# Kernel tuning notes

Hardware: AMD Instinct MI355X
Metric: run time of the kernel (lower is better)

Reference implementation:

```python
import jax, jax.numpy as jnp
import numpy as np


def setup_inputs() -> dict:
    key = jax.random.key(0)
    k1, k2, k3 = jax.random.split(key, 3)
    B, d, N, T = 8, 256, 4096, 1024
    K = jax.random.normal(k1, (B, d, N), dtype=jnp.float32)
    V = jax.random.normal(k2, (B, d, N), dtype=jnp.float32)
    Q = jax.random.normal(k3, (B, d, T), dtype=jnp.float32)
    return {"K": K, "V": V, "Q": Q}


def reference(K, V, Q):
    d = K.shape[1]
    scale = 1.0 / jnp.sqrt(jnp.asarray(d, dtype=K.dtype))
    # scores: (B, N, T) = K^T @ Q
    scores = jnp.einsum('bdn,bdt->bnt', K, Q) * scale
    A = jax.nn.softmax(scores, axis=1)  # softmax over keys N
    R = jnp.einsum('bdn,bnt->bdt', V, A)  # (B, d, T)
    R_ = jnp.concatenate((R, Q), axis=1)  # (B, 2d, T)
    maxAtt = jnp.argmax(A, axis=1)  # (B, T)
    return (R_, A, maxAtt)
```

## Files before the change

### kernel.cpp

```cpp
#include <hip/hip_runtime.h>
#include <cfloat>

#define BB 8
#define DD 256
#define NN 4096
#define TT 1024
constexpr float SCALE = 0.0625f;

typedef __attribute__((ext_vector_type(8))) short bf16x8;
typedef __attribute__((ext_vector_type(4))) float f32x4;
typedef __attribute__((ext_vector_type(8))) unsigned short u16x8;

__device__ inline unsigned short f2bf(float x) {
  union { float f; unsigned u; } v; v.f = x;
  unsigned r = v.u + 0x7fff + ((v.u >> 16) & 1);
  return (unsigned short)(r >> 16);
}
__device__ inline float bf2f(unsigned short h) {
  union { unsigned u; float f; } v; v.u = ((unsigned)h) << 16;
  return v.f;
}

__device__ inline void glds16(const unsigned short* g, const short* lbase) {
  __builtin_amdgcn_global_load_lds((const __attribute__((address_space(1))) unsigned int*)g,
                                   (__attribute__((address_space(3))) unsigned int*)lbase,
                                   16, 0, 0);
}

__device__ inline void wg_barrier() {
  __builtin_amdgcn_sched_barrier(0);
  __builtin_amdgcn_s_barrier();
  __builtin_amdgcn_sched_barrier(0);
}

#define MPART_OFF 0u
#define LPART_OFF (1u << 20)
#define IPART_OFF (2u << 20)
#define MARR_OFF  (3u << 20)
#define RLARR_OFF ((3u << 20) + 32768u)
#define CONV_OFF  (4u << 20)
#define KT_HI_OFF (CONV_OFF)
#define KT_LO_OFF (CONV_OFF + 16777216u)
#define QT_HI_OFF (CONV_OFF + 33554432u)
#define QT_LO_OFF (CONV_OFF + 37748736u)
#define VH_OFF    (CONV_OFF + 41943040u)
#define RPART_OFF (CONV_OFF)
#define WS_NEED   (62914560ull)

__global__ __launch_bounds__(256) void convert_t2(const float* __restrict__ Ksrc,
                                                  const float* __restrict__ Qsrc,
                                                  unsigned short* __restrict__ KHi,
                                                  unsigned short* __restrict__ KLo,
                                                  unsigned short* __restrict__ QHi,
                                                  unsigned short* __restrict__ QLo) {
  __shared__ float tile[64][65];
  const int bx = blockIdx.x;
  const int b = blockIdx.z, d0 = blockIdx.y * 64;
  const float* src; unsigned short* dhi; unsigned short* dlo; int C; int c0;
  if (bx < 64) { src = Ksrc; dhi = KHi; dlo = KLo; C = NN; c0 = bx * 64; }
  else         { src = Qsrc; dhi = QHi; dlo = QLo; C = TT; c0 = (bx - 64) * 64; }
  const int tid = threadIdx.x;
  const float* s = src + ((size_t)b * DD + d0) * C + c0;
  const int r = tid >> 4, cg = (tid & 15) * 4;
#pragma unroll
  for (int it = 0; it < 4; ++it) {
    float4 v = *(const float4*)(s + (size_t)(r + it * 16) * C + cg);
    tile[r + it * 16][cg + 0] = v.x; tile[r + it * 16][cg + 1] = v.y;
    tile[r + it * 16][cg + 2] = v.z; tile[r + it * 16][cg + 3] = v.w;
  }
  __syncthreads();
  const int cl = tid >> 2, dg = (tid & 3) * 16;
  unsigned short hi[16], lo[16];
#pragma unroll
  for (int j = 0; j < 16; ++j) {
    float x = tile[dg + j][cl];
    unsigned short h = f2bf(x);
    hi[j] = h;
    lo[j] = f2bf(x - bf2f(h));
  }
  size_t off = ((size_t)b * C + c0 + cl) * DD + d0 + dg;
  *(u16x8*)(dhi + off) = *(u16x8*)&hi[0];
  *(u16x8*)(dhi + off + 8) = *(u16x8*)&hi[8];
  *(u16x8*)(dlo + off) = *(u16x8*)&lo[0];
  *(u16x8*)(dlo + off + 8) = *(u16x8*)&lo[8];
}

__global__ __launch_bounds__(256) void convert_v(const float* __restrict__ src,
                                                 unsigned short* __restrict__ dhi) {
  size_t g = (size_t)blockIdx.x * 256 + threadIdx.x;
  float4 v = ((const float4*)src)[g];
  unsigned short h[4] = {f2bf(v.x), f2bf(v.y), f2bf(v.z), f2bf(v.w)};
  *(ushort4*)(dhi + g * 4) = *(ushort4*)h;
}

__global__ __launch_bounds__(256) void gemm_scores_mfma(const unsigned short* __restrict__ KtHi,
                                                        const unsigned short* __restrict__ KtLo,
                                                        const unsigned short* __restrict__ QtHi,
                                                        const unsigned short* __restrict__ QtLo,
                                                        float* __restrict__ S,
                                                        float* __restrict__ mPart,
                                                        float* __restrict__ lPart,
                                                        int* __restrict__ iPart) {
  __shared__ __align__(16) short sAhi[128 * 32];
  __shared__ __align__(16) short sAlo[128 * 32];
  __shared__ __align__(16) short sBhi[128 * 32];
  __shared__ __align__(16) short sBlo[128 * 32];
  __shared__ float sm[256], sl[256];
  __shared__ int si[256];

  const int lin = blockIdx.x + ((blockIdx.y + (blockIdx.z << 5)) << 3);
  const int wg = ((lin & 7) << 8) + (lin >> 3);
  const int b = wg >> 8;
  const int cy = (wg >> 3) & 31;
  const int n0 = cy * 128;
  const int t0 = (wg & 7) * 128;
  const int tid = threadIdx.x;
  const int lane = tid & 63, w = tid >> 6;
  const int nh = (w & 1) * 64, th = (w >> 1) * 64;
  const int fr = lane & 15, q = lane >> 4;

  const unsigned short* aHi = KtHi + ((size_t)b * NN + n0) * DD;
  const unsigned short* aLo = KtLo + ((size_t)b * NN + n0) * DD;
  const unsigned short* bHi = QtHi + ((size_t)b * TT + t0) * DD;
  const unsigned short* bLo = QtLo + ((size_t)b * TT + t0) * DD;

  f32x4 acc[4][4];
#pragma unroll
  for (int i = 0; i < 4; ++i)
#pragma unroll
    for (int j = 0; j < 4; ++j) acc[i][j] = (f32x4){0.f, 0.f, 0.f, 0.f};

  const int R = lane >> 2;
  const int Qq = (lane & 3) ^ ((lane >> 3) & 3);
  const size_t s0 = (size_t)((w * 2 + 0) * 16 + R) * DD + Qq * 8;
  const size_t s1 = (size_t)((w * 2 + 1) * 16 + R) * DD + Qq * 8;
  const int d0 = (w * 2 + 0) * 512;
  const int d1 = (w * 2 + 1) * 512;
  const int pq8 = (q ^ ((fr >> 1) & 3)) * 8;

  for (int kk = 0; kk < DD; kk += 32) {
    glds16(aHi + s0 + kk, sAhi + d0);
    glds16(aHi + s1 + kk, sAhi + d1);
    glds16(aLo + s0 + kk, sAlo + d0);
    glds16(aLo + s1 + kk, sAlo + d1);
    glds16(bHi + s0 + kk, sBhi + d0);
    glds16(bHi + s1 + kk, sBhi + d1);
    glds16(bLo + s0 + kk, sBlo + d0);
    glds16(bLo + s1 + kk, sBlo + d1);
    __syncthreads();

    bf16x8 bh[4], bl[4];
#pragma unroll
    for (int tb = 0; tb < 4; ++tb) {
      int off = (((w >> 1) * 4 + tb) * 512) + fr * 32 + pq8;
      bh[tb] = *(const bf16x8*)&sBhi[off];
      bl[tb] = *(const bf16x8*)&sBlo[off];
    }
#pragma unroll
    for (int mb = 0; mb < 4; ++mb) {
      int off = (((w & 1) * 4 + mb) * 512) + fr * 32 + pq8;
      bf16x8 ah = *(const bf16x8*)&sAhi[off];
      bf16x8 al = *(const bf16x8*)&sAlo[off];
#pragma unroll
      for (int tb = 0; tb < 4; ++tb) {
        acc[mb][tb] = __builtin_amdgcn_mfma_f32_16x16x32_bf16(ah, bh[tb], acc[mb][tb], 0, 0, 0);
        acc[mb][tb] = __builtin_amdgcn_mfma_f32_16x16x32_bf16(ah, bl[tb], acc[mb][tb], 0, 0, 0);
        acc[mb][tb] = __builtin_amdgcn_mfma_f32_16x16x32_bf16(al, bh[tb], acc[mb][tb], 0, 0, 0);
      }
    }
    __syncthreads();
  }

#pragma unroll
  for (int tb = 0; tb < 4; ++tb) {
    const int tl = th + tb * 16 + fr;
    const int t = t0 + tl;
    float tmp[16];
    float m = -FLT_MAX; int id = 0;
#pragma unroll
    for (int mb = 0; mb < 4; ++mb)
#pragma unroll
      for (int r = 0; r < 4; ++r) {
        float v = acc[mb][tb][r] * SCALE;
        int n = n0 + nh + mb * 16 + q * 4 + r;
        S[((size_t)b * NN + n) * TT + t] = v;
        tmp[mb * 4 + r] = v;
        int nl = nh + mb * 16 + q * 4 + r;
        if (v > m) { m = v; id = nl; }
      }
    float l = 0.f;
#pragma unroll
    for (int j = 0; j < 16; ++j) l += __expf(tmp[j] - m);
#pragma unroll
    for (int off = 16; off <= 32; off <<= 1) {
      float m2 = __shfl_xor(m, off);
      float l2 = __shfl_xor(l, off);
      int i2 = __shfl_xor(id, off);
      if (m2 > m)       { l = l * __expf(m - m2) + l2; m = m2; id = i2; }
      else if (m2 == m) { l += l2; id = min(id, i2); }
      else              { l += l2 * __expf(m2 - m); }
    }
    if (q == 0) {
      int slot = (w & 1) * 128 + tl;
      sm[slot] = m; sl[slot] = l; si[slot] = id;
    }
  }
  __syncthreads();
  if (tid < 128) {
    float m = sm[tid], l = sl[tid]; int id = si[tid];
    float m2 = sm[128 + tid], l2 = sl[128 + tid]; int i2 = si[128 + tid];
    if (m2 > m)       { l = l * __expf(m - m2) + l2; m = m2; id = i2; }
    else if (m2 == m) { l += l2; id = min(id, i2); }
    else              { l += l2 * __expf(m2 - m); }
    size_t p = ((size_t)b * 32 + cy) * TT + t0 + tid;
    mPart[p] = m; lPart[p] = l; iPart[p] = n0 + id;
  }
}

__global__ __launch_bounds__(256) void gemm_out_fused2(const unsigned short* __restrict__ Vh,
                                                       float* __restrict__ A,
                                                       const float* __restrict__ mPart,
                                                       const float* __restrict__ lPart,
                                                       const int* __restrict__ iPart,
                                                       float* __restrict__ Rpart,
                                                       float* __restrict__ outMax) {
  __shared__ __align__(16) short sV[2][256 * 32];
  __shared__ __align__(16) short sA[32 * 40];
  __shared__ float rsm[8][32], rsl[8][32];
  __shared__ int   rsi[8][32];
  __shared__ float sm[32], srl[32];

  const int lin = blockIdx.x + (blockIdx.y << 5) + (blockIdx.z << 7);
  const int b  = lin & 7;
  const int ny = (lin >> 3) & 3;
  const int t0 = ((lin >> 5) & 31) * 32;

  const int tid = threadIdx.x;
  const int lane = tid & 63, w = tid >> 6;
  const int fr = lane & 15, q = lane >> 4, fk = q * 8;
  const int sn = tid >> 3, tg = tid & 7;

  const unsigned short* Vb = Vh + (size_t)b * DD * NN;
  float* Ab = A + (size_t)b * NN * TT;
  float* Arow = Ab + (size_t)sn * TT + t0 + tg * 4;

  const int R = lane >> 2;
  const int Qq = (lane & 3) ^ ((lane >> 3) & 3);
  const unsigned short* vsrc = Vb + (size_t)(w * 64 + R) * NN + Qq * 8;
  const int pq8 = (q ^ ((fr >> 1) & 3)) * 8;
  const int n0 = ny * 1024;

#pragma unroll
  for (int c = 0; c < 4; ++c)
    glds16(vsrc + (size_t)(c * 16) * NN + n0, &sV[0][(w * 4 + c) * 512]);
  float4 cur = *(const float4*)(Arow + (size_t)n0 * TT);

  {
    const int tl = tid & 31, g = tid >> 5;
    float m = -FLT_MAX, l = 0.f; int idx = 0;
#pragma unroll
    for (int cc = 0; cc < 4; ++cc) {
      size_t p = ((size_t)b * 32 + g * 4 + cc) * TT + t0 + tl;
      float m2 = mPart[p], l2 = lPart[p]; int i2 = iPart[p];
      if (m2 > m)       { l = l * __expf(m - m2) + l2; m = m2; idx = i2; }
      else if (m2 == m) { l += l2; idx = min(idx, i2); }
      else              { l += l2 * __expf(m2 - m); }
    }
    rsm[g][tl] = m; rsl[g][tl] = l; rsi[g][tl] = idx;
  }
  __syncthreads();
  if (tid < 32) {
    float m = rsm[0][tid], l = rsl[0][tid]; int idx = rsi[0][tid];
#pragma unroll
    for (int g = 1; g < 8; ++g) {
      float m2 = rsm[g][tid], l2 = rsl[g][tid]; int i2 = rsi[g][tid];
      if (m2 > m)       { l = l * __expf(m - m2) + l2; m = m2; idx = i2; }
      else if (m2 == m) { l += l2; idx = min(idx, i2); }
      else              { l += l2 * __expf(m2 - m); }
    }
    sm[tid] = m; srl[tid] = 1.0f / l;
    if (ny == 0) outMax[(size_t)b * TT + t0 + tid] = (float)idx;
  }
  asm volatile("s_waitcnt vmcnt(0)" ::: "memory");
  __syncthreads();

  const float4 mv = *(const float4*)&sm[tg * 4];
  const float4 rv = *(const float4*)&srl[tg * 4];

  f32x4 acc[4][2];
#pragma unroll
  for (int i = 0; i < 4; ++i) { acc[i][0] = (f32x4){0,0,0,0}; acc[i][1] = (f32x4){0,0,0,0}; }

  for (int it = 0; it < 31; ++it) {
    const int nn = n0 + it * 32;
    const int bi = it & 1;
#pragma unroll
    for (int c = 0; c < 4; ++c)
      glds16(vsrc + (size_t)(c * 16) * NN + (nn + 32), &sV[bi ^ 1][(w * 4 + c) * 512]);
    float4 nxt = *(const float4*)(Arow + (size_t)(nn + 32) * TT);

    float4 av;
    av.x = __expf(cur.x - mv.x) * rv.x;
    av.y = __expf(cur.y - mv.y) * rv.y;
    av.z = __expf(cur.z - mv.z) * rv.z;
    av.w = __expf(cur.w - mv.w) * rv.w;
    *(float4*)(Arow + (size_t)nn * TT) = av;
    sA[(tg * 4 + 0) * 40 + sn] = (short)f2bf(av.x);
    sA[(tg * 4 + 1) * 40 + sn] = (short)f2bf(av.y);
    sA[(tg * 4 + 2) * 40 + sn] = (short)f2bf(av.z);
    sA[(tg * 4 + 3) * 40 + sn] = (short)f2bf(av.w);

    __builtin_amdgcn_sched_barrier(0);
    asm volatile("s_waitcnt vmcnt(8) lgkmcnt(0)" ::: "memory");
    wg_barrier();

    bf16x8 bf0 = *(const bf16x8*)&sA[(0 * 16 + fr) * 40 + fk];
    bf16x8 bf1 = *(const bf16x8*)&sA[(1 * 16 + fr) * 40 + fk];
#pragma unroll
    for (int mb = 0; mb < 4; ++mb) {
      bf16x8 af = *(const bf16x8*)&sV[bi][w * 2048 + mb * 512 + fr * 32 + pq8];
      acc[mb][0] = __builtin_amdgcn_mfma_f32_16x16x32_bf16(af, bf0, acc[mb][0], 0, 0, 0);
      acc[mb][1] = __builtin_amdgcn_mfma_f32_16x16x32_bf16(af, bf1, acc[mb][1], 0, 0, 0);
    }
    wg_barrier();
    cur = nxt;
  }

  {
    const int nn = n0 + 992;
    float4 av;
    av.x = __expf(cur.x - mv.x) * rv.x;
    av.y = __expf(cur.y - mv.y) * rv.y;
    av.z = __expf(cur.z - mv.z) * rv.z;
    av.w = __expf(cur.w - mv.w) * rv.w;
    *(float4*)(Arow + (size_t)nn * TT) = av;
    sA[(tg * 4 + 0) * 40 + sn] = (short)f2bf(av.x);
    sA[(tg * 4 + 1) * 40 + sn] = (short)f2bf(av.y);
    sA[(tg * 4 + 2) * 40 + sn] = (short)f2bf(av.z);
    sA[(tg * 4 + 3) * 40 + sn] = (short)f2bf(av.w);

    __builtin_amdgcn_sched_barrier(0);
    asm volatile("s_waitcnt vmcnt(0) lgkmcnt(0)" ::: "memory");
    wg_barrier();

    bf16x8 bf0 = *(const bf16x8*)&sA[(0 * 16 + fr) * 40 + fk];
    bf16x8 bf1 = *(const bf16x8*)&sA[(1 * 16 + fr) * 40 + fk];
#pragma unroll
    for (int mb = 0; mb < 4; ++mb) {
      bf16x8 af = *(const bf16x8*)&sV[1][w * 2048 + mb * 512 + fr * 32 + pq8];
      acc[mb][0] = __builtin_amdgcn_mfma_f32_16x16x32_bf16(af, bf0, acc[mb][0], 0, 0, 0);
      acc[mb][1] = __builtin_amdgcn_mfma_f32_16x16x32_bf16(af, bf1, acc[mb][1], 0, 0, 0);
    }
  }

#pragma unroll
  for (int mb = 0; mb < 4; ++mb)
#pragma unroll
    for (int tb = 0; tb < 2; ++tb) {
      const int t = t0 + tb * 16 + fr;
#pragma unroll
      for (int r = 0; r < 4; ++r) {
        const int d = w * 64 + mb * 16 + q * 4 + r;
        Rpart[(((size_t)b * 4 + ny) * DD + d) * TT + t] = acc[mb][tb][r];
      }
    }
}

__global__ __launch_bounds__(256) void combine(const float* __restrict__ Rpart,
                                               const float* __restrict__ Qp,
                                               float* __restrict__ out) {
  int g = blockIdx.x * 256 + threadIdx.x;
  int e = g * 4;
  int t = e & 1023;
  int row = e >> 10;
  int d = row & 511, b = row >> 9;
  if (d < 256) {
    float4 s0 = *(const float4*)(Rpart + (((size_t)b * 4 + 0) * DD + d) * TT + t);
    float4 s1 = *(const float4*)(Rpart + (((size_t)b * 4 + 1) * DD + d) * TT + t);
    float4 s2 = *(const float4*)(Rpart + (((size_t)b * 4 + 2) * DD + d) * TT + t);
    float4 s3 = *(const float4*)(Rpart + (((size_t)b * 4 + 3) * DD + d) * TT + t);
    float4 r = make_float4(s0.x + s1.x + s2.x + s3.x, s0.y + s1.y + s2.y + s3.y,
                           s0.z + s1.z + s2.z + s3.z, s0.w + s1.w + s2.w + s3.w);
    *(float4*)(out + ((size_t)b * 512 + d) * TT + t) = r;
  } else {
    float4 v = *(const float4*)(Qp + ((size_t)b * 256 + (d - 256)) * TT + t);
    *(float4*)(out + ((size_t)b * 512 + d) * TT + t) = v;
  }
}

__global__ __launch_bounds__(256) void gemm_scores_fp32(const float* __restrict__ Kp,
                                                        const float* __restrict__ Qp,
                                                        float* __restrict__ S) {
  const int b = blockIdx.z;
  const int n0 = blockIdx.y * 128;
  const int t0 = blockIdx.x * 128;
  const int tid = threadIdx.x;
  const int tx = tid & 15, ty = tid >> 4;
  __shared__ float Kt[8][128];
  __shared__ float Qt[8][128];
  float acc[8][8];
#pragma unroll
  for (int i = 0; i < 8; ++i)
#pragma unroll
    for (int j = 0; j < 8; ++j) acc[i][j] = 0.f;
  const int lin = tid * 4;
  const int lkk = lin >> 7, lcol = lin & 127;
  const float* Kbase = Kp + (size_t)b * DD * NN;
  const float* Qbase = Qp + (size_t)b * DD * TT;
  for (int dd0 = 0; dd0 < DD; dd0 += 8) {
    float4 kv = *(const float4*)(Kbase + (size_t)(dd0 + lkk) * NN + n0 + lcol);
    float4 qv = *(const float4*)(Qbase + (size_t)(dd0 + lkk) * TT + t0 + lcol);
    __syncthreads();
    *(float4*)&Kt[lkk][lcol] = kv;
    *(float4*)&Qt[lkk][lcol] = qv;
    __syncthreads();
#pragma unroll
    for (int kk = 0; kk < 8; ++kk) {
      float4 a0 = *(float4*)&Kt[kk][ty * 4];
      float4 a1 = *(float4*)&Kt[kk][64 + ty * 4];
      float4 b0 = *(float4*)&Qt[kk][tx * 4];
      float4 b1 = *(float4*)&Qt[kk][64 + tx * 4];
      float av[8] = {a0.x, a0.y, a0.z, a0.w, a1.x, a1.y, a1.z, a1.w};
      float bv[8] = {b0.x, b0.y, b0.z, b0.w, b1.x, b1.y, b1.z, b1.w};
#pragma unroll
      for (int i = 0; i < 8; ++i)
#pragma unroll
        for (int j = 0; j < 8; ++j) acc[i][j] += av[i] * bv[j];
    }
  }
#pragma unroll
  for (int i = 0; i < 8; ++i) {
    int r = n0 + ((i < 4) ? (ty * 4 + i) : (64 + ty * 4 + i - 4));
    float* dst = S + ((size_t)b * NN + r) * TT + t0;
    *(float4*)(dst + tx * 4) = make_float4(acc[i][0] * SCALE, acc[i][1] * SCALE, acc[i][2] * SCALE, acc[i][3] * SCALE);
    *(float4*)(dst + 64 + tx * 4) = make_float4(acc[i][4] * SCALE, acc[i][5] * SCALE, acc[i][6] * SCALE, acc[i][7] * SCALE);
  }
}

__global__ __launch_bounds__(256) void stats_partial_fb(const float* __restrict__ S,
                                                        float* __restrict__ mPart,
                                                        float* __restrict__ lPart,
                                                        int* __restrict__ iPart) {
  const int tid = threadIdx.x;
  const int tx = tid & 63, ty = tid >> 6;
  const int b = blockIdx.z;
  const int t = blockIdx.x * 64 + tx;
  const int nbase = blockIdx.y * 512;
  float m = -FLT_MAX, l = 0.f;
  int idx = 0;
  const float* col = S + (size_t)b * NN * TT + t;
  for (int n = nbase + ty; n < nbase + 512; n += 4) {
    float s = col[(size_t)n * TT];
    if (s > m) { l = l * __expf(m - s) + 1.0f; m = s; idx = n; }
    else        l += __expf(s - m);
  }
  __shared__ float sm[4][64], sl[4][64];
  __shared__ int si[4][64];
  sm[ty][tx] = m; sl[ty][tx] = l; si[ty][tx] = idx;
  __syncthreads();
  if (ty == 0) {
#pragma unroll
    for (int k = 1; k < 4; ++k) {
      float m2 = sm[k][tx], l2 = sl[k][tx];
      int i2 = si[k][tx];
      if (m2 > m)       { l = l * __expf(m - m2) + l2; m = m2; idx = i2; }
      else if (m2 == m) { l += l2; idx = min(idx, i2); }
      else              { l += l2 * __expf(m2 - m); }
    }
    size_t p = (size_t)(b * 8 + blockIdx.y) * TT + t;
    mPart[p] = m; lPart[p] = l; iPart[p] = idx;
  }
}

__global__ __launch_bounds__(256) void stats_final_fb(const float* __restrict__ mPart,
                                                      const float* __restrict__ lPart,
                                                      const int* __restrict__ iPart,
                                                      float* __restrict__ mArr,
                                                      float* __restrict__ rlArr,
                                                      float* __restrict__ outMax) {
  int col = blockIdx.x * 256 + threadIdx.x;
  int b = col >> 10, t = col & 1023;
  float m = -FLT_MAX, l = 0.f;
  int idx = 0;
#pragma unroll
  for (int c = 0; c < 8; ++c) {
    size_t p = (size_t)(b * 8 + c) * TT + t;
    float m2 = mPart[p], l2 = lPart[p];
    int i2 = iPart[p];
    if (m2 > m)       { l = l * __expf(m - m2) + l2; m = m2; idx = i2; }
    else if (m2 == m) { l += l2; idx = min(idx, i2); }
    else              { l += l2 * __expf(m2 - m); }
  }
  mArr[col] = m;
  rlArr[col] = 1.0f / l;
  outMax[col] = (float)idx;
}

__global__ __launch_bounds__(256) void normalize_fb(float* __restrict__ A,
                                                    const float* __restrict__ mArr,
                                                    const float* __restrict__ rlArr) {
  int g = blockIdx.x * 256 + threadIdx.x;
  float4 s = ((const float4*)A)[g];
  int e = g * 4;
  int t0 = e & 1023;
  int row = e >> 10;
  int b = row >> 12;
  int cb = (b << 10) + t0;
  float4 r;
  r.x = __expf(s.x - mArr[cb + 0]) * rlArr[cb + 0];
  r.y = __expf(s.y - mArr[cb + 1]) * rlArr[cb + 1];
  r.z = __expf(s.z - mArr[cb + 2]) * rlArr[cb + 2];
  r.w = __expf(s.w - mArr[cb + 3]) * rlArr[cb + 3];
  ((float4*)A)[g] = r;
}

__global__ __launch_bounds__(256) void gemm_out_fp32(const float* __restrict__ Vp,
                                                     const float* __restrict__ A,
                                                     float* __restrict__ Rout) {
  const int b = blockIdx.z;
  const int m0 = blockIdx.y * 64;
  const int t0 = blockIdx.x * 128;
  const int tid = threadIdx.x;
  const int tx = tid & 15, ty = tid >> 4;
  __shared__ float Vt[16][68];
  __shared__ float At[16][128];
  float acc[4][8];
#pragma unroll
  for (int i = 0; i < 4; ++i)
#pragma unroll
    for (int j = 0; j < 8; ++j) acc[i][j] = 0.f;
  const float* Vbase = Vp + (size_t)b * DD * NN;
  const float* Abase = A + (size_t)b * NN * TT;
  const int vmm = tid >> 2, vkk = (tid & 3) * 4;
  const int akk = tid >> 5, att = (tid * 4) & 127;
  for (int nn0 = 0; nn0 < NN; nn0 += 16) {
    float4 vv = *(const float4*)(Vbase + (size_t)(m0 + vmm) * NN + nn0 + vkk);
    float4 a0 = *(const float4*)(Abase + (size_t)(nn0 + akk) * TT + t0 + att);
    float4 a1 = *(const float4*)(Abase + (size_t)(nn0 + akk + 8) * TT + t0 + att);
    __syncthreads();
    Vt[vkk + 0][vmm] = vv.x; Vt[vkk + 1][vmm] = vv.y;
    Vt[vkk + 2][vmm] = vv.z; Vt[vkk + 3][vmm] = vv.w;
    *(float4*)&At[akk][att] = a0;
    *(float4*)&At[akk + 8][att] = a1;
    __syncthreads();
#pragma unroll
    for (int kk = 0; kk < 16; ++kk) {
      float4 a4 = *(float4*)&Vt[kk][ty * 4];
      float4 b0 = *(float4*)&At[kk][tx * 4];
      float4 b1 = *(float4*)&At[kk][64 + tx * 4];
      float av[4] = {a4.x, a4.y, a4.z, a4.w};
      float bv[8] = {b0.x, b0.y, b0.z, b0.w, b1.x, b1.y, b1.z, b1.w};
#pragma unroll
      for (int i = 0; i < 4; ++i)
#pragma unroll
        for (int j = 0; j < 8; ++j) acc[i][j] += av[i] * bv[j];
    }
  }
#pragma unroll
  for (int i = 0; i < 4; ++i) {
    int r = m0 + ty * 4 + i;
    float* dst = Rout + (size_t)b * (2 * DD) * TT + (size_t)r * TT + t0;
    *(float4*)(dst + tx * 4) = make_float4(acc[i][0], acc[i][1], acc[i][2], acc[i][3]);
    *(float4*)(dst + 64 + tx * 4) = make_float4(acc[i][4], acc[i][5], acc[i][6], acc[i][7]);
  }
}

__global__ __launch_bounds__(256) void qcopy(const float* __restrict__ Qp,
                                             float* __restrict__ out) {
  int g = blockIdx.x * 256 + threadIdx.x;
  int e = g * 4;
  int t0 = e & 1023;
  int row = e >> 10;
  int dd = row & 255, b = row >> 8;
  float4 v = ((const float4*)Qp)[g];
  *(float4*)(out + (size_t)b * 512 * TT + (size_t)(256 + dd) * TT + t0) = v;
}

extern "C" void kernel_launch(void* const* d_in, const int* in_sizes, int n_in,
                              void* d_out, int out_size, void* d_ws, size_t ws_size,
                              hipStream_t stream) {
  const float* Kp = (const float*)d_in[0];
  const float* Vp = (const float*)d_in[1];
  const float* Qp = (const float*)d_in[2];
  float* out = (float*)d_out;
  float* R_ = out;
  float* A = out + 4194304;
  float* outMax = out + 4194304 + 33554432;

  char* wsb = (char*)d_ws;
  float* mPart = (float*)(wsb + MPART_OFF);
  float* lPart = (float*)(wsb + LPART_OFF);
  int*   iPart = (int*)(wsb + IPART_OFF);
  float* mArr  = (float*)(wsb + MARR_OFF);
  float* rlArr = (float*)(wsb + RLARR_OFF);

  const bool fast = (ws_size >= WS_NEED);

  if (fast) {
    unsigned short* KtHi = (unsigned short*)(wsb + KT_HI_OFF);
    unsigned short* KtLo = (unsigned short*)(wsb + KT_LO_OFF);
    unsigned short* QtHi = (unsigned short*)(wsb + QT_HI_OFF);
    unsigned short* QtLo = (unsigned short*)(wsb + QT_LO_OFF);
    unsigned short* Vh   = (unsigned short*)(wsb + VH_OFF);
    float* Rpart = (float*)(wsb + RPART_OFF);

    convert_t2<<<dim3(80, 4, BB), 256, 0, stream>>>(Kp, Qp, KtHi, KtLo, QtHi, QtLo);
    convert_v<<<dim3((BB * DD * NN / 4) / 256), 256, 0, stream>>>(Vp, Vh);
    gemm_scores_mfma<<<dim3(TT / 128, NN / 128, BB), 256, 0, stream>>>(
        KtHi, KtLo, QtHi, QtLo, A, mPart, lPart, iPart);
    gemm_out_fused2<<<dim3(TT / 32, 4, BB), 256, 0, stream>>>(
        Vh, A, mPart, lPart, iPart, Rpart, outMax);
    combine<<<dim3((BB * 512 * TT / 4) / 256), 256, 0, stream>>>(Rpart, Qp, R_);
  } else {
    gemm_scores_fp32<<<dim3(TT / 128, NN / 128, BB), 256, 0, stream>>>(Kp, Qp, A);
    stats_partial_fb<<<dim3(TT / 64, NN / 512, BB), 256, 0, stream>>>(A, mPart, lPart, iPart);
    stats_final_fb<<<dim3(32), 256, 0, stream>>>(mPart, lPart, iPart, mArr, rlArr, outMax);
    normalize_fb<<<dim3((BB * NN * TT / 4) / 256), 256, 0, stream>>>(A, mArr, rlArr);
    gemm_out_fp32<<<dim3(TT / 128, DD / 64, BB), 256, 0, stream>>>(Vp, A, R_);
    qcopy<<<dim3((BB * DD * TT / 4) / 256), 256, 0, stream>>>(Qp, R_);
  }
}
```

Baseline: 334.2 us.

## Double-buffer score GEMM LDS loads, merge conversion kernels, remap combine blocks

The score GEMM now stages the next K-slice into a second LDS buffer with global_load_lds while computing on the current one, using explicit vmcnt waits and workgroup barriers in place of a load-then-sync loop. The K/Q transpose-split conversion and the V bf16 conversion are merged into one launch to save a kernel launch and let the two run concurrently. The combine kernel is remapped so each block handles one (b, d) row with batch interleaved across adjacent blocks. Double buffering doubles the GEMM's LDS footprint, which may reduce occupancy.

Measured after the change: 328.4 us. About the same (-1.7%).

```diff
diff --git a/kernel.cpp b/kernel.cpp
--- a/kernel.cpp
+++ b/kernel.cpp
@@ -47,19 +47,32 @@
 #define RPART_OFF (CONV_OFF)
 #define WS_NEED   (62914560ull)
 
-__global__ __launch_bounds__(256) void convert_t2(const float* __restrict__ Ksrc,
-                                                  const float* __restrict__ Qsrc,
-                                                  unsigned short* __restrict__ KHi,
-                                                  unsigned short* __restrict__ KLo,
-                                                  unsigned short* __restrict__ QHi,
-                                                  unsigned short* __restrict__ QLo) {
+__global__ __launch_bounds__(256) void convert_all(const float* __restrict__ Ksrc,
+                                                   const float* __restrict__ Qsrc,
+                                                   const float* __restrict__ Vsrc,
+                                                   unsigned short* __restrict__ KHi,
+                                                   unsigned short* __restrict__ KLo,
+                                                   unsigned short* __restrict__ QHi,
+                                                   unsigned short* __restrict__ QLo,
+                                                   unsigned short* __restrict__ Vh) {
   __shared__ float tile[64][65];
   const int bx = blockIdx.x;
-  const int b = blockIdx.z, d0 = blockIdx.y * 64;
+  const int b = blockIdx.z;
+  const int tid = threadIdx.x;
+
+  if (bx >= 80) {
+    const int y = blockIdx.y;
+    size_t g = (((size_t)b * 4 + y) * 256 + (bx - 80)) * 256 + tid;
+    float4 v = ((const float4*)Vsrc)[g];
+    unsigned short h[4] = {f2bf(v.x), f2bf(v.y), f2bf(v.z), f2bf(v.w)};
+    *(ushort4*)(Vh + g * 4) = *(ushort4*)h;
+    return;
+  }
+
+  const int d0 = blockIdx.y * 64;
   const float* src; unsigned short* dhi; unsigned short* dlo; int C; int c0;
   if (bx < 64) { src = Ksrc; dhi = KHi; dlo = KLo; C = NN; c0 = bx * 64; }
   else         { src = Qsrc; dhi = QHi; dlo = QLo; C = TT; c0 = (bx - 64) * 64; }
-  const int tid = threadIdx.x;
   const float* s = src + ((size_t)b * DD + d0) * C + c0;
   const int r = tid >> 4, cg = (tid & 15) * 4;
 #pragma unroll
@@ -83,14 +96,6 @@
   *(u16x8*)(dhi + off + 8) = *(u16x8*)&hi[8];
   *(u16x8*)(dlo + off) = *(u16x8*)&lo[0];
   *(u16x8*)(dlo + off + 8) = *(u16x8*)&lo[8];
-}
-
-__global__ __launch_bounds__(256) void convert_v(const float* __restrict__ src,
-                                                 unsigned short* __restrict__ dhi) {
-  size_t g = (size_t)blockIdx.x * 256 + threadIdx.x;
-  float4 v = ((const float4*)src)[g];
-  unsigned short h[4] = {f2bf(v.x), f2bf(v.y), f2bf(v.z), f2bf(v.w)};
-  *(ushort4*)(dhi + g * 4) = *(ushort4*)h;
 }
 
 __global__ __launch_bounds__(256) void gemm_scores_mfma(const unsigned short* __restrict__ KtHi,
@@ -101,10 +106,10 @@
                                                         float* __restrict__ mPart,
                                                         float* __restrict__ lPart,
                                                         int* __restrict__ iPart) {
-  __shared__ __align__(16) short sAhi[128 * 32];
-  __shared__ __align__(16) short sAlo[128 * 32];
-  __shared__ __align__(16) short sBhi[128 * 32];
-  __shared__ __align__(16) short sBlo[128 * 32];
+  __shared__ __align__(16) short sAhi[2][128 * 32];
+  __shared__ __align__(16) short sAlo[2][128 * 32];
+  __shared__ __align__(16) short sBhi[2][128 * 32];
+  __shared__ __align__(16) short sBlo[2][128 * 32];
   __shared__ float sm[256], sl[256];
   __shared__ int si[256];
 
@@ -130,37 +135,50 @@
 #pragma unroll
     for (int j = 0; j < 4; ++j) acc[i][j] = (f32x4){0.f, 0.f, 0.f, 0.f};
 
-  const int R = lane >> 2;
+  const int Rr = lane >> 2;
   const int Qq = (lane & 3) ^ ((lane >> 3) & 3);
-  const size_t s0 = (size_t)((w * 2 + 0) * 16 + R) * DD + Qq * 8;
-  const size_t s1 = (size_t)((w * 2 + 1) * 16 + R) * DD + Qq * 8;
-  const int d0 = (w * 2 + 0) * 512;
-  const int d1 = (w * 2 + 1) * 512;
+  const size_t s0 = (size_t)((w * 2 + 0) * 16 + Rr) * DD + Qq * 8;
+  const size_t s1 = (size_t)((w * 2 + 1) * 16 + Rr) * DD + Qq * 8;
+  const int g0 = (w * 2 + 0) * 512;
+  const int g1 = (w * 2 + 1) * 512;
   const int pq8 = (q ^ ((fr >> 1) & 3)) * 8;
 
-  for (int kk = 0; kk < DD; kk += 32) {
-    glds16(aHi + s0 + kk, sAhi + d0);
-    glds16(aHi + s1 + kk, sAhi + d1);
-    glds16(aLo + s0 + kk, sAlo + d0);
-    glds16(aLo + s1 + kk, sAlo + d1);
-    glds16(bHi + s0 + kk, sBhi + d0);
-    glds16(bHi + s1 + kk, sBhi + d1);
-    glds16(bLo + s0 + kk, sBlo + d0);
-    glds16(bLo + s1 + kk, sBlo + d1);
-    __syncthreads();
+#define STAGE_K1(buf, kk)                         \
+    glds16(aHi + s0 + (kk), &sAhi[buf][g0]);      \
+    glds16(aHi + s1 + (kk), &sAhi[buf][g1]);      \
+    glds16(aLo + s0 + (kk), &sAlo[buf][g0]);      \
+    glds16(aLo + s1 + (kk), &sAlo[buf][g1]);      \
+    glds16(bHi + s0 + (kk), &sBhi[buf][g0]);      \
+    glds16(bHi + s1 + (kk), &sBhi[buf][g1]);      \
+    glds16(bLo + s0 + (kk), &sBlo[buf][g0]);      \
+    glds16(bLo + s1 + (kk), &sBlo[buf][g1]);
+
+  STAGE_K1(0, 0);
+
+  for (int step = 0; step < 8; ++step) {
+    const int bi = step & 1;
+    if (step < 7) {
+      STAGE_K1(bi ^ 1, (step + 1) * 32);
+      __builtin_amdgcn_sched_barrier(0);
+      asm volatile("s_waitcnt vmcnt(8)" ::: "memory");
+    } else {
+      __builtin_amdgcn_sched_barrier(0);
+      asm volatile("s_waitcnt vmcnt(0)" ::: "memory");
+    }
+    wg_barrier();
 
     bf16x8 bh[4], bl[4];
 #pragma unroll
     for (int tb = 0; tb < 4; ++tb) {
       int off = (((w >> 1) * 4 + tb) * 512) + fr * 32 + pq8;
-      bh[tb] = *(const bf16x8*)&sBhi[off];
-      bl[tb] = *(const bf16x8*)&sBlo[off];
+      bh[tb] = *(const bf16x8*)&sBhi[bi][off];
+      bl[tb] = *(const bf16x8*)&sBlo[bi][off];
     }
 #pragma unroll
     for (int mb = 0; mb < 4; ++mb) {
       int off = (((w & 1) * 4 + mb) * 512) + fr * 32 + pq8;
-      bf16x8 ah = *(const bf16x8*)&sAhi[off];
-      bf16x8 al = *(const bf16x8*)&sAlo[off];
+      bf16x8 ah = *(const bf16x8*)&sAhi[bi][off];
+      bf16x8 al = *(const bf16x8*)&sAlo[bi][off];
 #pragma unroll
       for (int tb = 0; tb < 4; ++tb) {
         acc[mb][tb] = __builtin_amdgcn_mfma_f32_16x16x32_bf16(ah, bh[tb], acc[mb][tb], 0, 0, 0);
@@ -168,8 +186,9 @@
         acc[mb][tb] = __builtin_amdgcn_mfma_f32_16x16x32_bf16(al, bh[tb], acc[mb][tb], 0, 0, 0);
       }
     }
-    __syncthreads();
-  }
+    wg_barrier();
+  }
+#undef STAGE_K1
 
 #pragma unroll
   for (int tb = 0; tb < 4; ++tb) {
@@ -244,9 +263,9 @@
   float* Ab = A + (size_t)b * NN * TT;
   float* Arow = Ab + (size_t)sn * TT + t0 + tg * 4;
 
-  const int R = lane >> 2;
+  const int Rr = lane >> 2;
   const int Qq = (lane & 3) ^ ((lane >> 3) & 3);
-  const unsigned short* vsrc = Vb + (size_t)(w * 64 + R) * NN + Qq * 8;
+  const unsigned short* vsrc = Vb + (size_t)(w * 64 + Rr) * NN + Qq * 8;
   const int pq8 = (q ^ ((fr >> 1) & 3)) * 8;
   const int n0 = ny * 1024;
 
@@ -369,11 +388,10 @@
 __global__ __launch_bounds__(256) void combine(const float* __restrict__ Rpart,
                                                const float* __restrict__ Qp,
                                                float* __restrict__ out) {
-  int g = blockIdx.x * 256 + threadIdx.x;
-  int e = g * 4;
-  int t = e & 1023;
-  int row = e >> 10;
-  int d = row & 511, b = row >> 9;
+  const int lin = blockIdx.x;
+  const int b = lin & 7;
+  const int d = lin >> 3;
+  const int t = threadIdx.x * 4;
   if (d < 256) {
     float4 s0 = *(const float4*)(Rpart + (((size_t)b * 4 + 0) * DD + d) * TT + t);
     float4 s1 = *(const float4*)(Rpart + (((size_t)b * 4 + 1) * DD + d) * TT + t);
@@ -604,13 +622,12 @@
     unsigned short* Vh   = (unsigned short*)(wsb + VH_OFF);
     float* Rpart = (float*)(wsb + RPART_OFF);
 
-    convert_t2<<<dim3(80, 4, BB), 256, 0, stream>>>(Kp, Qp, KtHi, KtLo, QtHi, QtLo);
-    convert_v<<<dim3((BB * DD * NN / 4) / 256), 256, 0, stream>>>(Vp, Vh);
+    convert_all<<<dim3(336, 4, BB), 256, 0, stream>>>(Kp, Qp, Vp, KtHi, KtLo, QtHi, QtLo, Vh);
     gemm_scores_mfma<<<dim3(TT / 128, NN / 128, BB), 256, 0, stream>>>(
         KtHi, KtLo, QtHi, QtLo, A, mPart, lPart, iPart);
     gemm_out_fused2<<<dim3(TT / 32, 4, BB), 256, 0, stream>>>(
         Vh, A, mPart, lPart, iPart, Rpart, outMax);
-    combine<<<dim3((BB * 512 * TT / 4) / 256), 256, 0, stream>>>(Rpart, Qp, R_);
+    combine<<<dim3(4096), 256, 0, stream>>>(Rpart, Qp, R_);
   } else {
     gemm_scores_fp32<<<dim3(TT / 128, NN / 128, BB), 256, 0, stream>>>(Kp, Qp, A);
     stats_partial_fb<<<dim3(TT / 64, NN / 512, BB), 256, 0, stream>>>(A, mPart, lPart, iPart);
```
